# Performance work log

Measured on AMD Instinct MI355X. Metric: run time of the kernel, lower is better.

The kernel has to match this reference:

```python
import jax, jax.numpy as jnp
import numpy as np

EPS = 1e-9


def setup_inputs() -> dict:
    key = jax.random.key(0)
    k1, k2, k3 = jax.random.split(key, 3)
    B, N, E, F_IN, F_OUT = 8, 2048, 1024, 256, 256
    x = jax.random.normal(k1, (B, N, F_IN), dtype=jnp.float32)
    H = jax.random.uniform(k2, (B, N, E), dtype=jnp.float32)  # soft incidence matrix
    weight = jax.random.normal(k3, (F_IN, F_OUT), dtype=jnp.float32) * (1.0 / np.sqrt(F_OUT))
    return {"x": x, "H": H, "weight": weight}


def reference(x, H, weight):
    # x: [B, N, Fin], H: [B, N, E], weight: [Fin, Fout]
    # Torch builds diag_embed(Dv_inv)/diag_embed(De_inv) and uses dense bmm;
    # mathematically identical to elementwise row-scaling, done here directly.
    Dv = jnp.sum(H, axis=2)                       # [B, N]  (= bmm(H, ones))
    De = jnp.sum(H, axis=1)                       # [B, E]
    Dv_inv = 1.0 / (Dv + EPS)
    De_inv = 1.0 / (De + EPS)
    xw = jnp.matmul(x, weight)                    # [B, N, Fout]
    HTX = jnp.einsum('bne,bnf->bef', H, xw)       # H^T @ X
    HDeHTX = jnp.einsum('bne,bef->bnf', H, De_inv[:, :, None] * HTX)
    out = Dv_inv[:, :, None] * HDeHTX             # [B, N, Fout]
    # dropout in eval mode (identity); relu kept
    return jax.nn.relu(out)
```

## Files before the change

### kernel.cpp

```cpp
#include <hip/hip_runtime.h>
#include <stdint.h>


typedef __bf16 bf16x8 __attribute__((ext_vector_type(8)));
typedef float f32x4 __attribute__((ext_vector_type(4)));

__device__ __forceinline__ uint16_t f2b(float f) {
  __bf16 h = (__bf16)f;
  return __builtin_bit_cast(uint16_t, h);
}

__device__ __forceinline__ f32x4 mfma16(bf16x8 a, bf16x8 b, f32x4 c) {
  return __builtin_amdgcn_mfma_f32_16x16x32_bf16(a, b, c, 0, 0, 0);
}

__device__ __forceinline__ void gload16(const void* src, void* dst) {
  __builtin_amdgcn_global_load_lds(
      (const __attribute__((address_space(1))) void*)src,
      (__attribute__((address_space(3))) void*)dst, 16, 0, 0);
}

#define PIPE_WAIT4() do { \
    asm volatile("s_waitcnt vmcnt(4)" ::: "memory"); \
    __builtin_amdgcn_s_barrier(); \
    __builtin_amdgcn_sched_barrier(0); \
  } while (0)
#define PIPE_WAIT0() do { \
    asm volatile("s_waitcnt vmcnt(0)" ::: "memory"); \
    __builtin_amdgcn_s_barrier(); \
    __builtin_amdgcn_sched_barrier(0); \
  } while (0)

__global__ __launch_bounds__(256) void k_prep_w(const float* __restrict__ W,
    uint16_t* __restrict__ Wt) {
  __shared__ __align__(16) uint16_t T[64 * 68];
  const int k0 = blockIdx.x * 64, f0 = blockIdx.y * 64;
  const int t = threadIdx.x;
  const int r0 = (t >> 4) * 4, cc = (t & 15) * 4;
  float vv[4][4];
  #pragma unroll
  for (int i = 0; i < 4; ++i) {
    float4 q = *(const float4*)(W + (size_t)(k0 + r0 + i) * 256 + f0 + cc);
    vv[i][0] = q.x; vv[i][1] = q.y; vv[i][2] = q.z; vv[i][3] = q.w;
  }
  #pragma unroll
  for (int j = 0; j < 4; ++j) {
    union { uint16_t s[4]; uint2 u; } p;
    #pragma unroll
    for (int i = 0; i < 4; ++i) p.s[i] = f2b(vv[i][j]);
    *(uint2*)&T[(cc + j) * 68 + r0] = p.u;
  }
  __syncthreads();
  const int er = t >> 2, c2 = (t & 3) * 16;
  union { uint16_t s[16]; uint4 q[2]; } o;
  #pragma unroll
  for (int m = 0; m < 4; ++m)
    *(uint2*)&o.s[m * 4] = *(const uint2*)&T[er * 68 + c2 + m * 4];
  uint16_t* dst = Wt + (size_t)(f0 + er) * 256 + k0 + c2;
  *(uint4*)dst = o.q[0];
  *(uint4*)(dst + 8) = o.q[1];
}

__global__ __launch_bounds__(256) void k_phase1(const float* __restrict__ H,
    const float* __restrict__ X, const uint16_t* __restrict__ Wt,
    uint16_t* __restrict__ Hb, float* __restrict__ DvInv,
    float* __restrict__ DePart, uint16_t* __restrict__ XWt) {
  __shared__ __align__(16) unsigned char smem[17408];
  const int lin = blockIdx.x;
  const int t = threadIdx.x, lane = t & 63, wave = t >> 6;

  if (lin < 1024) {
    float* dvp = (float*)smem;
    const int nb = lin & 127, b = lin >> 7;
    const int n0 = nb * 16;
    const float* Hrow = H + ((size_t)b * 2048 + n0) * 1024 + t * 4;
    uint16_t* HbRow = Hb + ((size_t)b * 2048 + n0) * 1024 + t * 4;
    float de0 = 0.f, de1 = 0.f, de2 = 0.f, de3 = 0.f;
    float4 qn = *(const float4*)(Hrow);
    #pragma unroll
    for (int i = 0; i < 16; ++i) {
      float4 q = qn;
      if (i < 15) qn = *(const float4*)(Hrow + (size_t)(i + 1) * 1024);
      de0 += q.x; de1 += q.y; de2 += q.z; de3 += q.w;
      float rs = (q.x + q.y) + (q.z + q.w);
      rs += __shfl_xor(rs, 1);  rs += __shfl_xor(rs, 2);
      rs += __shfl_xor(rs, 4);  rs += __shfl_xor(rs, 8);
      rs += __shfl_xor(rs, 16); rs += __shfl_xor(rs, 32);
      if (lane == 0) dvp[i * 4 + wave] = rs;
      union { uint16_t s[4]; uint2 u; } p;
      p.s[0] = f2b(q.x); p.s[1] = f2b(q.y); p.s[2] = f2b(q.z); p.s[3] = f2b(q.w);
      *(uint2*)(HbRow + (size_t)i * 1024) = p.u;
    }
    {
      float* dp = DePart + ((size_t)b * 1024 + t * 4) * 128 + nb;
      dp[0] = de0; dp[128] = de1; dp[256] = de2; dp[384] = de3;
    }
    __syncthreads();
    if (t < 16) {
      float s = (dvp[t * 4 + 0] + dvp[t * 4 + 1]) + (dvp[t * 4 + 2] + dvp[t * 4 + 3]);
      DvInv[b * 2048 + n0 + t] = 1.f / (s + 1e-9f);
    }
  } else {
    uint16_t* As = (uint16_t*)smem;
    uint16_t* Bs = (uint16_t*)(smem + 8192);
    const int l1 = lin - 1024;
    const int n0 = (l1 & 31) * 64, f0 = ((l1 >> 5) & 3) * 64, b = l1 >> 7;
    const int l15 = lane & 15, lq = lane >> 4;
    const int rlane = lane >> 3;
    const int srcswz = ((lane & 7) ^ rlane) << 3;
    const uint16_t* Ag = Wt + (size_t)f0 * 256;
    const int br = t >> 2, kc = (t & 3) * 16;
    const float* Xg = X + ((size_t)b * 2048 + n0 + br) * 256 + kc;
    f32x4 acc[2][2] = {};
    for (int kt = 0; kt < 4; ++kt) {
      if (kt) __syncthreads();
      const int k0 = kt * 64;
      #pragma unroll
      for (int i = 0; i < 2; ++i) {
        const int r = wave * 16 + i * 8;
        gload16(Ag + (size_t)(r + rlane) * 256 + k0 + srcswz, As + r * 64);
      }
      {
        float4 RX[4];
        const float* s = Xg + k0;
        #pragma unroll
        for (int q = 0; q < 4; ++q) RX[q] = *(const float4*)(s + q * 4);
        uint16_t* d = Bs + br * 72 + kc;
        const float* f = (const float*)RX;
        #pragma unroll
        for (int q = 0; q < 2; ++q) {
          union { uint16_t s[8]; uint4 u; } p;
          #pragma unroll
          for (int j = 0; j < 8; ++j) p.s[j] = f2b(f[q * 8 + j]);
          *(uint4*)(d + q * 8) = p.u;
        }
      }
      __syncthreads();
      #pragma unroll
      for (int h = 0; h < 2; ++h) {
        bf16x8 af[2], bf[2];
        #pragma unroll
        for (int i = 0; i < 2; ++i) {
          const int r = (wave >> 1) * 32 + i * 16 + l15;
          af[i] = *(const bf16x8*)(As + r * 64 + ((((h << 2) | lq) ^ (r & 7)) << 3));
        }
        #pragma unroll
        for (int j = 0; j < 2; ++j) {
          const int r = (wave & 1) * 32 + j * 16 + l15;
          bf[j] = *(const bf16x8*)(Bs + r * 72 + h * 32 + lq * 8);
        }
        #pragma unroll
        for (int i = 0; i < 2; ++i)
          #pragma unroll
          for (int j = 0; j < 2; ++j)
            acc[i][j] = mfma16(af[i], bf[j], acc[i][j]);
      }
    }
    #pragma unroll
    for (int i = 0; i < 2; ++i) {
      const int fr = f0 + (wave >> 1) * 32 + i * 16 + lq * 4;
      #pragma unroll
      for (int j = 0; j < 2; ++j) {
        const int col = n0 + (wave & 1) * 32 + j * 16 + l15;
        #pragma unroll
        for (int reg = 0; reg < 4; ++reg)
          XWt[((size_t)b * 256 + fr + reg) * 2048 + col] = f2b(acc[i][j][reg]);
      }
    }
  }
}

__global__ __launch_bounds__(256) void k_gemm2(const uint16_t* __restrict__ Hb,
    const uint16_t* __restrict__ XWt, const float* __restrict__ DePart,
    uint16_t* __restrict__ Yt) {
  __shared__ __align__(16) uint16_t As[3][64 * 64];
  __shared__ __align__(16) uint16_t Bsm[2][64 * 72];
  __shared__ float sde4[64][4];
  __shared__ float sde[64];
  const int e0 = blockIdx.x * 64, f0 = blockIdx.y * 64, b = blockIdx.z;
  const int t = threadIdx.x, lane = t & 63, wave = t >> 6;
  const int l15 = lane & 15, lq = lane >> 4;
  const int rlane = lane >> 3;
  const int srcswz = ((lane & 7) ^ rlane) << 3;
  const uint16_t* Ag = XWt + ((size_t)b * 256 + f0) * 2048;
  const int br0 = (t >> 4) * 4;
  const int bcc = (t & 15) * 4;
  const uint16_t* Bgb = Hb + (size_t)b * 2048 * 1024 + e0 + bcc;
  auto stageA = [&](uint16_t* Ad, int kt) {
    const int k0 = kt * 64;
    #pragma unroll
    for (int i = 0; i < 2; ++i) {
      const int r = wave * 16 + i * 8;
      gload16(Ag + (size_t)(r + rlane) * 2048 + k0 + srcswz, Ad + r * 64);
    }
  };
  auto loadB = [&](uint2* R, int kt) {
    const uint16_t* s = Bgb + (size_t)(kt * 64 + br0) * 1024;
    #pragma unroll
    for (int i = 0; i < 4; ++i) R[i] = *(const uint2*)(s + (size_t)i * 1024);
  };
  auto writeB = [&](uint16_t* Bd, const uint2* R) {
    #pragma unroll
    for (int j = 0; j < 4; ++j) {
      union { uint16_t s[4]; uint2 u; } p;
      #pragma unroll
      for (int i = 0; i < 4; ++i) p.s[i] = ((const uint16_t*)&R[i])[j];
      *(uint2*)&Bd[(bcc + j) * 72 + br0] = p.u;
    }
  };
  f32x4 acc[2][2] = {};
  auto compute = [&](const uint16_t* Ad, const uint16_t* Bd) {
    #pragma unroll
    for (int h = 0; h < 2; ++h) {
      bf16x8 af[2], bf[2];
      #pragma unroll
      for (int i = 0; i < 2; ++i) {
        const int r = (wave >> 1) * 32 + i * 16 + l15;
        af[i] = *(const bf16x8*)(Ad + r * 64 + ((((h << 2) | lq) ^ (r & 7)) << 3));
      }
      #pragma unroll
      for (int j = 0; j < 2; ++j) {
        const int r = (wave & 1) * 32 + j * 16 + l15;
        bf[j] = *(const bf16x8*)(Bd + r * 72 + h * 32 + lq * 8);
      }
      #pragma unroll
      for (int i = 0; i < 2; ++i)
        #pragma unroll
        for (int j = 0; j < 2; ++j)
          acc[i][j] = mfma16(af[i], bf[j], acc[i][j]);
    }
  };
  {
    const float* p = DePart + ((size_t)b * 1024 + e0 + (t & 63)) * 128 + (t >> 6) * 32;
    float s = 0.f;
    #pragma unroll
    for (int q = 0; q < 8; ++q) {
      float4 a = *(const float4*)(p + q * 4);
      s += (a.x + a.y) + (a.z + a.w);
    }
    sde4[t & 63][t >> 6] = s;
  }
  uint2 RB0[4], RB1[4];
  loadB(RB0, 0);
  stageA(As[0], 0);
  stageA(As[1], 1);
  asm volatile("s_waitcnt vmcnt(4)" ::: "memory");
  writeB(Bsm[0], RB0);
  loadB(RB1, 1);
  asm volatile("s_waitcnt vmcnt(6) lgkmcnt(0)" ::: "memory");
  __builtin_amdgcn_s_barrier();
  __builtin_amdgcn_sched_barrier(0);
  if (t < 64)
    sde[t] = 1.f / (((sde4[t][0] + sde4[t][1]) + (sde4[t][2] + sde4[t][3])) + 1e-9f);
  const int NT = 32;
  uint16_t *cA = As[0], *nA = As[1], *fA = As[2];
  #define G2_STEP(KT, RBH, RBF, BSC, BSN)                                    \
    do {                                                                     \
      stageA(fA, (KT) + 2);                                                  \
      loadB(RBF, (KT) + 2);                                                  \
      compute(cA, BSC);                                                      \
      asm volatile("s_waitcnt vmcnt(6)" ::: "memory");                       \
      writeB(BSN, RBH);                                                      \
      asm volatile("s_waitcnt lgkmcnt(0)" ::: "memory");                     \
      __builtin_amdgcn_s_barrier();                                          \
      __builtin_amdgcn_sched_barrier(0);                                     \
      uint16_t* tp = cA; cA = nA; nA = fA; fA = tp;                          \
    } while (0)
  for (int kt = 0; kt < NT - 2; kt += 2) {
    G2_STEP(kt,     RB1, RB0, Bsm[0], Bsm[1]);
    G2_STEP(kt + 1, RB0, RB1, Bsm[1], Bsm[0]);
  }
  #undef G2_STEP
  compute(cA, Bsm[0]);
  asm volatile("s_waitcnt vmcnt(0)" ::: "memory");
  writeB(Bsm[1], RB1);
  asm volatile("s_waitcnt lgkmcnt(0)" ::: "memory");
  __builtin_amdgcn_s_barrier();
  __builtin_amdgcn_sched_barrier(0);
  compute(nA, Bsm[1]);
  #pragma unroll
  for (int i = 0; i < 2; ++i) {
    const int fr = f0 + (wave >> 1) * 32 + i * 16 + lq * 4;
    #pragma unroll
    for (int j = 0; j < 2; ++j) {
      const int el = (wave & 1) * 32 + j * 16 + l15;
      const float sc = sde[el];
      uint16_t* dst = Yt + ((size_t)b * 256 + fr) * 1024 + e0 + el;
      #pragma unroll
      for (int reg = 0; reg < 4; ++reg)
        dst[(size_t)reg * 1024] = f2b(acc[i][j][reg] * sc);
    }
  }
}

__global__ __launch_bounds__(256) void k_gemm3(const uint16_t* __restrict__ Hb,
    const uint16_t* __restrict__ Yt, const float* __restrict__ DvInv,
    float* __restrict__ out) {
  __shared__ __align__(16) uint16_t As[3][64 * 64];
  __shared__ __align__(16) uint16_t Bs[3][64 * 64];
  __shared__ float sdv[64];
  const int n0 = blockIdx.x * 64, f0 = blockIdx.y * 64, b = blockIdx.z;
  const int t = threadIdx.x, lane = t & 63, wave = t >> 6;
  const int l15 = lane & 15, lq = lane >> 4;
  const int rlane = lane >> 3;
  const int srcswz = ((lane & 7) ^ rlane) << 3;
  const uint16_t* Ag = Hb + ((size_t)b * 2048 + n0) * 1024;
  const uint16_t* Bg = Yt + ((size_t)b * 256 + f0) * 1024;
  auto stage = [&](uint16_t* Ad, uint16_t* Bd, int kt) {
    const int k0 = kt * 64;
    #pragma unroll
    for (int i = 0; i < 2; ++i) {
      const int r = wave * 16 + i * 8;
      gload16(Ag + (size_t)(r + rlane) * 1024 + k0 + srcswz, Ad + r * 64);
      gload16(Bg + (size_t)(r + rlane) * 1024 + k0 + srcswz, Bd + r * 64);
    }
  };
  f32x4 acc[2][2] = {};
  auto compute = [&](const uint16_t* Ad, const uint16_t* Bd) {
    #pragma unroll
    for (int h = 0; h < 2; ++h) {
      bf16x8 af[2], bf[2];
      #pragma unroll
      for (int i = 0; i < 2; ++i) {
        const int r = (wave >> 1) * 32 + i * 16 + l15;
        af[i] = *(const bf16x8*)(Ad + r * 64 + ((((h << 2) | lq) ^ (r & 7)) << 3));
      }
      #pragma unroll
      for (int j = 0; j < 2; ++j) {
        const int r = (wave & 1) * 32 + j * 16 + l15;
        bf[j] = *(const bf16x8*)(Bd + r * 64 + ((((h << 2) | lq) ^ (r & 7)) << 3));
      }
      #pragma unroll
      for (int i = 0; i < 2; ++i)
        #pragma unroll
        for (int j = 0; j < 2; ++j)
          acc[i][j] = mfma16(af[i], bf[j], acc[i][j]);
    }
  };
  if (t < 64) sdv[t] = DvInv[b * 2048 + n0 + t];
  stage(As[0], Bs[0], 0);
  stage(As[1], Bs[1], 1);
  __syncthreads();
  const int NT = 16;
  uint16_t *cA = As[0], *nA = As[1], *fA = As[2];
  uint16_t *cB = Bs[0], *nB = Bs[1], *fB = Bs[2];
  for (int kt = 0; kt < NT - 2; ++kt) {
    stage(fA, fB, kt + 2);
    compute(cA, cB);
    PIPE_WAIT4();
    uint16_t* t1 = cA; cA = nA; nA = fA; fA = t1;
    uint16_t* t2 = cB; cB = nB; nB = fB; fB = t2;
  }
  compute(cA, cB);
  PIPE_WAIT0();
  compute(nA, nB);
  #pragma unroll
  for (int i = 0; i < 2; ++i) {
    const int nl = (wave >> 1) * 32 + i * 16 + lq * 4;
    #pragma unroll
    for (int reg = 0; reg < 4; ++reg) {
      const int row = n0 + nl + reg;
      const float sc = sdv[nl + reg];
      #pragma unroll
      for (int j = 0; j < 2; ++j) {
        const int col = f0 + (wave & 1) * 32 + j * 16 + l15;
        const float v = acc[i][j][reg] * sc;
        out[((size_t)b * 2048 + row) * 256 + col] = v > 0.f ? v : 0.f;
      }
    }
  }
}

extern "C" void kernel_launch(void* const* d_in, const int* in_sizes, int n_in,
                              void* d_out, int out_size, void* d_ws, size_t ws_size,
                              hipStream_t stream) {
  (void)in_sizes; (void)n_in; (void)out_size;
  const float* x = (const float*)d_in[0];
  const float* H = (const float*)d_in[1];
  const float* W = (const float*)d_in[2];
  float* out = (float*)d_out;

  if (ws_size < 50528256) return;
  char* ws = (char*)d_ws;
  uint16_t* Hb     = (uint16_t*)(ws);
  uint16_t* XWt    = (uint16_t*)(ws + 33554432);
  uint16_t* Yt     = (uint16_t*)(ws + 41943040);
  float*    DvInv  = (float*)(ws + 46137344);
  float*    DePart = (float*)(ws + 46202880);
  uint16_t* Wt     = (uint16_t*)(ws + 50397184);

  k_prep_w<<<dim3(4, 4),     256, 0, stream>>>(W, Wt);
  k_phase1<<<dim3(2048),     256, 0, stream>>>(H, x, Wt, Hb, DvInv, DePart, XWt);
  k_gemm2 <<<dim3(16, 4, 8), 256, 0, stream>>>(Hb, XWt, DePart, Yt);
  k_gemm3 <<<dim3(32, 4, 8), 256, 0, stream>>>(Hb, Yt, DvInv, out);
}
```

Measured before the change: 88.44 us.

## Transpose DePart layout for coalesced stores and batch H loads in groups of four

The per-block partial column sums of H (DePart) now use a [b][nb][e] layout. Phase 1 can then write them as one coalesced float4 per thread instead of four scattered scalar stores strided by 128 floats. The consumer in phase 2 switches to coalesced strided scalar reads over 32 partials. The H row loads are also regrouped into batches of four independent float4 loads, replacing the one-ahead prefetch, to expose more memory-level parallelism. This costs more registers and scalar rather than vector reads on the consumer side.

```diff
diff --git a/kernel.cpp b/kernel.cpp
--- a/kernel.cpp
+++ b/kernel.cpp
@@ -76,25 +76,29 @@
     const float* Hrow = H + ((size_t)b * 2048 + n0) * 1024 + t * 4;
     uint16_t* HbRow = Hb + ((size_t)b * 2048 + n0) * 1024 + t * 4;
     float de0 = 0.f, de1 = 0.f, de2 = 0.f, de3 = 0.f;
-    float4 qn = *(const float4*)(Hrow);
-    #pragma unroll
-    for (int i = 0; i < 16; ++i) {
-      float4 q = qn;
-      if (i < 15) qn = *(const float4*)(Hrow + (size_t)(i + 1) * 1024);
-      de0 += q.x; de1 += q.y; de2 += q.z; de3 += q.w;
-      float rs = (q.x + q.y) + (q.z + q.w);
-      rs += __shfl_xor(rs, 1);  rs += __shfl_xor(rs, 2);
-      rs += __shfl_xor(rs, 4);  rs += __shfl_xor(rs, 8);
-      rs += __shfl_xor(rs, 16); rs += __shfl_xor(rs, 32);
-      if (lane == 0) dvp[i * 4 + wave] = rs;
-      union { uint16_t s[4]; uint2 u; } p;
-      p.s[0] = f2b(q.x); p.s[1] = f2b(q.y); p.s[2] = f2b(q.z); p.s[3] = f2b(q.w);
-      *(uint2*)(HbRow + (size_t)i * 1024) = p.u;
-    }
-    {
-      float* dp = DePart + ((size_t)b * 1024 + t * 4) * 128 + nb;
-      dp[0] = de0; dp[128] = de1; dp[256] = de2; dp[384] = de3;
-    }
+    #pragma unroll
+    for (int g = 0; g < 4; ++g) {
+      float4 q[4];
+      #pragma unroll
+      for (int i = 0; i < 4; ++i)
+        q[i] = *(const float4*)(Hrow + (size_t)(g * 4 + i) * 1024);
+      #pragma unroll
+      for (int i = 0; i < 4; ++i) {
+        const int r = g * 4 + i;
+        de0 += q[i].x; de1 += q[i].y; de2 += q[i].z; de3 += q[i].w;
+        float rs = (q[i].x + q[i].y) + (q[i].z + q[i].w);
+        rs += __shfl_xor(rs, 1);  rs += __shfl_xor(rs, 2);
+        rs += __shfl_xor(rs, 4);  rs += __shfl_xor(rs, 8);
+        rs += __shfl_xor(rs, 16); rs += __shfl_xor(rs, 32);
+        if (lane == 0) dvp[r * 4 + wave] = rs;
+        union { uint16_t s[4]; uint2 u; } p;
+        p.s[0] = f2b(q[i].x); p.s[1] = f2b(q[i].y);
+        p.s[2] = f2b(q[i].z); p.s[3] = f2b(q[i].w);
+        *(uint2*)(HbRow + (size_t)r * 1024) = p.u;
+      }
+    }
+    *(float4*)(DePart + ((size_t)b * 128 + nb) * 1024 + t * 4) =
+        make_float4(de0, de1, de2, de3);
     __syncthreads();
     if (t < 16) {
       float s = (dvp[t * 4 + 0] + dvp[t * 4 + 1]) + (dvp[t * 4 + 2] + dvp[t * 4 + 3]);
@@ -231,13 +235,11 @@
     }
   };
   {
-    const float* p = DePart + ((size_t)b * 1024 + e0 + (t & 63)) * 128 + (t >> 6) * 32;
+    const float* p = DePart + (size_t)b * 128 * 1024 + (t >> 6) * 32 * 1024
+                   + e0 + (t & 63);
     float s = 0.f;
     #pragma unroll
-    for (int q = 0; q < 8; ++q) {
-      float4 a = *(const float4*)(p + q * 4);
-      s += (a.x + a.y) + (a.z + a.w);
-    }
+    for (int q = 0; q < 32; ++q) s += p[(size_t)q * 1024];
     sde4[t & 63][t >> 6] = s;
   }
   uint2 RB0[4], RB1[4];
```

Measured after the change: 82.14 us. -7.1%, faster.
